# Kernel optimization log

Hardware: AMD Instinct MI355X
Metric: run time of the kernel (lower is better)

The kernel has to match this reference:

```python
import jax, jax.numpy as jnp
import numpy as np
from jax.ops import segment_sum

IN_DIM, HID_DIM, OUT_DIM = 128, 128, 64
N_NODES, N_EDGES = 50000, 800000


def gcn_conv(x, src, dst, W, b, n_nodes):
    # Symmetric GCN normalization (no self loops): deg at targets from unit weights
    deg = segment_sum(jnp.ones(src.shape[0], dtype=x.dtype), dst, num_segments=n_nodes)
    dinv = jnp.where(deg > 0, jax.lax.rsqrt(jnp.maximum(deg, 1.0)), 0.0)
    norm = dinv[src] * dinv[dst]                      # [E]
    h = x @ W                                         # [N, out] small GEMM first (PyG order)
    msg = h[src] * norm[:, None]                      # gather + scale: [E, out]
    out = segment_sum(msg, dst, num_segments=n_nodes) # scatter-add to targets
    return out + b


def setup_inputs() -> dict:
    key = jax.random.key(0)
    k1, k2, k3, k4, k5 = jax.random.split(key, 5)
    x = jax.random.normal(k1, (N_NODES, IN_DIM), dtype=jnp.float32)
    edge_index = jax.random.randint(k2, (2, N_EDGES), 0, N_NODES, dtype=jnp.int64)
    s1 = 1.0 / np.sqrt(IN_DIM)
    s2 = 1.0 / np.sqrt(HID_DIM)
    W1 = jax.random.uniform(k3, (IN_DIM, HID_DIM), jnp.float32, -s1, s1)
    b1 = jnp.zeros((HID_DIM,), jnp.float32)
    W2 = jax.random.uniform(k4, (HID_DIM, OUT_DIM), jnp.float32, -s2, s2)
    b2 = jnp.zeros((OUT_DIM,), jnp.float32)
    return {"x": x, "edge_index": edge_index, "W1": W1, "b1": b1, "W2": W2, "b2": b2}


def reference(x, edge_index, W1, b1, W2, b2):
    n_nodes = x.shape[0]
    src, dst = edge_index[0], edge_index[1]
    h = gcn_conv(x, src, dst, W1, b1, n_nodes)
    h = jax.nn.relu(h)
    # Dropout is identity in eval mode (reference is deterministic)
    out = gcn_conv(h, src, dst, W2, b2, n_nodes)
    return out
```

## Files before the change

kernel.cpp:

```cpp
#include <hip/hip_runtime.h>

#define N_NODES 50000
#define N_EDGES 800000
#define IN_DIM  128
#define HID_DIM 128
#define OUT_DIM 64

#define NPAD 50176
#define NB 7
#define KEYS (N_NODES * NB)
#define KPAD 350208
#define NB_SCAN2 (KPAD / 1024)
#define FILLB ((N_EDGES / 4 + 255) / 256)
#define DINVB ((N_NODES + 1023) / 1024)
#define GEMM1B1024 (NPAD / 256)
#define RANKB (N_EDGES / 256)
#define PREPB 24

typedef __attribute__((ext_vector_type(8))) short bf16x8;
typedef __attribute__((ext_vector_type(4))) float f32x4;

__device__ __forceinline__ unsigned short f2bf(float f) {
    unsigned u = __float_as_uint(f);
    u += 0x7fffu + ((u >> 16) & 1u);
    return (unsigned short)(u >> 16);
}
__device__ __forceinline__ float bflo(unsigned u) { return __uint_as_float(u << 16); }
__device__ __forceinline__ float bfhi(unsigned u) { return __uint_as_float(u & 0xffff0000u); }

#define ACC8(u)  do { \
    acc[0] += bflo(u.x); acc[1] += bfhi(u.x); \
    acc[2] += bflo(u.y); acc[3] += bfhi(u.y); \
    acc[4] += bflo(u.z); acc[5] += bfhi(u.z); \
    acc[6] += bflo(u.w); acc[7] += bfhi(u.w); } while (0)

#define FMA8(u, sc_)  do { \
    acc[0] += bflo(u.x) * (sc_); acc[1] += bfhi(u.x) * (sc_); \
    acc[2] += bflo(u.y) * (sc_); acc[3] += bfhi(u.y) * (sc_); \
    acc[4] += bflo(u.z) * (sc_); acc[5] += bfhi(u.z) * (sc_); \
    acc[6] += bflo(u.w) * (sc_); acc[7] += bfhi(u.w) * (sc_); } while (0)


__global__ __launch_bounds__(256) void prep_rank_kernel(const int* __restrict__ src,
                                                        const int* __restrict__ dst,
                                                        int* __restrict__ cnt2,
                                                        int* __restrict__ rank,
                                                        const float* __restrict__ W1,
                                                        const float* __restrict__ W2,
                                                        unsigned short* __restrict__ w1t,
                                                        unsigned short* __restrict__ w2t) {
    int bid = blockIdx.x;
    int tid = threadIdx.x;
    if (bid < 16) {
        int idx = bid * 256 + tid;
        int c = idx >> 5, k4 = (idx & 31) * 4;
        ushort4 o;
        o.x = f2bf(W1[(k4 + 0) * 128 + c]);
        o.y = f2bf(W1[(k4 + 1) * 128 + c]);
        o.z = f2bf(W1[(k4 + 2) * 128 + c]);
        o.w = f2bf(W1[(k4 + 3) * 128 + c]);
        *(ushort4*)(w1t + c * 128 + k4) = o;
    } else if (bid < PREPB) {
        int idx = (bid - 16) * 256 + tid;
        int c = idx >> 5, k4 = (idx & 31) * 4;
        ushort4 o;
        o.x = f2bf(W2[(k4 + 0) * 64 + c]);
        o.y = f2bf(W2[(k4 + 1) * 64 + c]);
        o.z = f2bf(W2[(k4 + 2) * 64 + c]);
        o.w = f2bf(W2[(k4 + 3) * 64 + c]);
        *(ushort4*)(w2t + c * 128 + k4) = o;
    } else {
        int e = (bid - PREPB) * 256 + tid;
        int s = src[e], d = dst[e];
        rank[e] = atomicAdd(&cnt2[d * NB + (s >> 13)], 1);
    }
}


__global__ __launch_bounds__(1024) void scan_dinv_gemm1_kernel(const int* __restrict__ cnt2,
                                                               int* __restrict__ partials,
                                                               int* __restrict__ rs,
                                                               float* __restrict__ dinv,
                                                               const float* __restrict__ x,
                                                               const unsigned short* __restrict__ w1t,
                                                               unsigned short* __restrict__ h1b) {
    int bid = blockIdx.x;
    int tid = threadIdx.x;
    if (bid < NB_SCAN2) {
        __shared__ int wsum[16];
        __shared__ int woffE[16];
        __shared__ int psum[16];
        __shared__ int bpre;
        int lane = tid & 63, wid = tid >> 6;
        int i = bid * 1024 + tid;
        int v = (i < KEYS) ? cnt2[i] : 0;
        int s = v;
#pragma unroll
        for (int off = 1; off < 64; off <<= 1) {
            int t = __shfl_up(s, off, 64);
            if (lane >= off) s += t;
        }
        if (lane == 63) wsum[wid] = s;
        __syncthreads();
        if (wid == 0) {
            int ws = (lane < 16) ? wsum[lane] : 0;
            int wi = ws;
#pragma unroll
            for (int off = 1; off < 16; off <<= 1) {
                int t = __shfl_up(wi, off, 64);
                if (lane >= off) wi += t;
            }
            if (lane < 16) woffE[lane] = wi - ws;
            if (lane == 15) atomicExch(&partials[bid], wi + 1);
        }
        if (bid == 0 && tid == 0) rs[KEYS] = N_EDGES;
        int myp = 0;
        if (tid < bid) {
            int val;
            do { val = atomicAdd(&partials[tid], 0); } while (val == 0);
            myp = val - 1;
        }
#pragma unroll
        for (int d = 1; d < 64; d <<= 1) myp += __shfl_xor(myp, d, 64);
        if (lane == 0) psum[wid] = myp;
        __syncthreads();
        if (tid == 0) {
            int b = 0;
#pragma unroll
            for (int t = 0; t < 16; ++t) b += psum[t];
            bpre = b;
        }
        __syncthreads();
        if (i < KEYS) rs[i] = bpre + woffE[wid] + s - v;
    } else if (bid < NB_SCAN2 + DINVB) {
        int d = (bid - NB_SCAN2) * 1024 + tid;
        if (d < N_NODES) {
            int base = d * NB;
            int deg = cnt2[base] + cnt2[base + 1] + cnt2[base + 2] + cnt2[base + 3]
                    + cnt2[base + 4] + cnt2[base + 5] + cnt2[base + 6];
            dinv[d] = (deg > 0) ? rsqrtf((float)deg) : 0.0f;
        }
    } else {
        int gb = bid - NB_SCAN2 - DINVB;
        int wave = tid >> 6;
        int lane = tid & 63;
        int n = lane & 15, quad = lane >> 4;
        int row0 = gb * 256 + wave * 16;

        int arow = row0 + n;
        if (arow >= N_NODES) arow = N_NODES - 1;
        const float* aptr = x + (size_t)arow * 128 + quad * 8;
        const unsigned short* bbase = w1t + (size_t)n * 128 + quad * 8;

        f32x4 acc[8];
#pragma unroll
        for (int t = 0; t < 8; ++t) acc[t] = (f32x4){0.f, 0.f, 0.f, 0.f};

#pragma unroll
        for (int w4 = 0; w4 < 4; ++w4) {
            float4 f0 = *(const float4*)(aptr + w4 * 32);
            float4 f1 = *(const float4*)(aptr + w4 * 32 + 4);
            bf16x8 af;
            af[0] = (short)f2bf(f0.x); af[1] = (short)f2bf(f0.y);
            af[2] = (short)f2bf(f0.z); af[3] = (short)f2bf(f0.w);
            af[4] = (short)f2bf(f1.x); af[5] = (short)f2bf(f1.y);
            af[6] = (short)f2bf(f1.z); af[7] = (short)f2bf(f1.w);
#pragma unroll
            for (int t = 0; t < 8; ++t) {
                bf16x8 bf = *(const bf16x8*)(bbase + (size_t)t * 2048 + w4 * 32);
                acc[t] = __builtin_amdgcn_mfma_f32_16x16x32_bf16(af, bf, acc[t], 0, 0, 0);
            }
        }

#pragma unroll
        for (int r = 0; r < 4; ++r) {
            int row = row0 + quad * 4 + r;
            if (row < N_NODES) {
                unsigned short* o = h1b + (size_t)row * 128 + n;
#pragma unroll
                for (int t = 0; t < 8; ++t) o[t * 16] = f2bf(acc[t][r]);
            }
        }
    }
}


__global__ __launch_bounds__(256) void fill_kernel(const int* __restrict__ src,
                                                   const int* __restrict__ dst,
                                                   const int* __restrict__ rank,
                                                   const int* __restrict__ rs,
                                                   int* __restrict__ csr_src) {
    int e = (blockIdx.x * 256 + threadIdx.x) * 4;
    if (e >= N_EDGES) return;
    int4 s4 = *(const int4*)(src + e);
    int4 d4 = *(const int4*)(dst + e);
    int4 r4 = *(const int4*)(rank + e);
    csr_src[rs[d4.x * NB + (s4.x >> 13)] + r4.x] = s4.x;
    csr_src[rs[d4.y * NB + (s4.y >> 13)] + r4.y] = s4.y;
    csr_src[rs[d4.z * NB + (s4.z >> 13)] + r4.z] = s4.z;
    csr_src[rs[d4.w * NB + (s4.w >> 13)] + r4.w] = s4.w;
}


#define A1T_STRIDE 136

__global__ __launch_bounds__(256) void agg1_gemm2_fused(const int* __restrict__ csr_src,
                                                        const int* __restrict__ rs,
                                                        const float* __restrict__ dinv,
                                                        const float* __restrict__ b1,
                                                        const unsigned short* __restrict__ h1b,
                                                        const unsigned short* __restrict__ w2t,
                                                        unsigned short* __restrict__ h2b) {
    __shared__ unsigned short a1t[16 * A1T_STRIDE];

    int node0 = blockIdx.x * 16;
    int g = threadIdx.x >> 4;
    int q = threadIdx.x & 15;
    int node = node0 + g;
    int start = rs[node * NB];
    int m = rs[node * NB + NB] - start;

    float acc[8] = {};
    int j = 0;
    for (; j + 3 < m; j += 4) {
        int s0 = csr_src[start + j];
        int s1 = csr_src[start + j + 1];
        int s2 = csr_src[start + j + 2];
        int s3 = csr_src[start + j + 3];
        float ds0 = dinv[s0];
        float ds1 = dinv[s1];
        float ds2 = dinv[s2];
        float ds3 = dinv[s3];
        uint4 u0 = ((const uint4*)(h1b + (size_t)s0 * 128))[q];
        uint4 u1 = ((const uint4*)(h1b + (size_t)s1 * 128))[q];
        uint4 u2 = ((const uint4*)(h1b + (size_t)s2 * 128))[q];
        uint4 u3 = ((const uint4*)(h1b + (size_t)s3 * 128))[q];
        FMA8(u0, ds0); FMA8(u1, ds1); FMA8(u2, ds2); FMA8(u3, ds3);
    }
    for (; j < m; ++j) {
        int s0 = csr_src[start + j];
        float ds0 = dinv[s0];
        uint4 u0 = ((const uint4*)(h1b + (size_t)s0 * 128))[q];
        FMA8(u0, ds0);
    }

    {
        float dn = dinv[node];
        float4 bA = ((const float4*)b1)[2 * q];
        float4 bB = ((const float4*)b1)[2 * q + 1];
        ushort4 oA, oB;
        oA.x = f2bf(fmaxf(acc[0] * dn + bA.x, 0.f));
        oA.y = f2bf(fmaxf(acc[1] * dn + bA.y, 0.f));
        oA.z = f2bf(fmaxf(acc[2] * dn + bA.z, 0.f));
        oA.w = f2bf(fmaxf(acc[3] * dn + bA.w, 0.f));
        oB.x = f2bf(fmaxf(acc[4] * dn + bB.x, 0.f));
        oB.y = f2bf(fmaxf(acc[5] * dn + bB.y, 0.f));
        oB.z = f2bf(fmaxf(acc[6] * dn + bB.z, 0.f));
        oB.w = f2bf(fmaxf(acc[7] * dn + bB.w, 0.f));
        ushort4* o = (ushort4*)(a1t + g * A1T_STRIDE + q * 8);
        o[0] = oA;
        o[1] = oB;
    }
    __syncthreads();

    int wave = threadIdx.x >> 6;
    int lane = threadIdx.x & 63;
    int n = lane & 15, quad = lane >> 4;
    const unsigned short* bbase = w2t + (size_t)(wave * 16 + n) * 128 + quad * 8;
    const unsigned short* abase = a1t + (size_t)n * A1T_STRIDE + quad * 8;

    f32x4 c2 = (f32x4){0.f, 0.f, 0.f, 0.f};
#pragma unroll
    for (int w4 = 0; w4 < 4; ++w4) {
        bf16x8 af = *(const bf16x8*)(abase + w4 * 32);
        bf16x8 bf = *(const bf16x8*)(bbase + w4 * 32);
        c2 = __builtin_amdgcn_mfma_f32_16x16x32_bf16(af, bf, c2, 0, 0, 0);
    }

#pragma unroll
    for (int r = 0; r < 4; ++r) {
        int row = node0 + quad * 4 + r;
        float dn = dinv[row];
        h2b[(size_t)row * 64 + wave * 16 + n] = f2bf(c2[r] * dn);
    }
}


__global__ __launch_bounds__(256) void agg2_kernel(const int* __restrict__ csr_src,
                                                   const int* __restrict__ rs,
                                                   const float* __restrict__ dinv,
                                                   const float* __restrict__ b2,
                                                   const unsigned short* __restrict__ h2b,
                                                   float* __restrict__ out) {
    int node = blockIdx.x * 4 + (threadIdx.x >> 6);
    if (node >= N_NODES) return;
    int lane = threadIdx.x & 63;
    int grp = lane >> 3;
    int q   = lane & 7;
    int start = rs[node * NB];
    int m = rs[node * NB + NB] - start;

    float acc[8] = {};

    int j = grp;
    for (; j + 8 < m; j += 16) {
        int s0 = csr_src[start + j];
        int s1 = csr_src[start + j + 8];
        uint4 u0 = ((const uint4*)(h2b + (size_t)s0 * 64))[q];
        uint4 u1 = ((const uint4*)(h2b + (size_t)s1 * 64))[q];
        ACC8(u0); ACC8(u1);
    }
    if (j < m) {
        int s0 = csr_src[start + j];
        uint4 u0 = ((const uint4*)(h2b + (size_t)s0 * 64))[q];
        ACC8(u0);
    }

#pragma unroll
    for (int d = 8; d <= 32; d <<= 1) {
#pragma unroll
        for (int c = 0; c < 8; ++c) acc[c] += __shfl_xor(acc[c], d, 64);
    }

    if (lane < 8) {
        float dn = dinv[node];
        float4 bA = ((const float4*)b2)[2 * q];
        float4 bB = ((const float4*)b2)[2 * q + 1];
        float4 rA, rB;
        rA.x = acc[0] * dn + bA.x;
        rA.y = acc[1] * dn + bA.y;
        rA.z = acc[2] * dn + bA.z;
        rA.w = acc[3] * dn + bA.w;
        rB.x = acc[4] * dn + bB.x;
        rB.y = acc[5] * dn + bB.y;
        rB.z = acc[6] * dn + bB.z;
        rB.w = acc[7] * dn + bB.w;
        float4* o = (float4*)(out + (size_t)node * 64);
        o[2 * q] = rA;
        o[2 * q + 1] = rB;
    }
}


extern "C" void kernel_launch(void* const* d_in, const int* in_sizes, int n_in,
                              void* d_out, int out_size, void* d_ws, size_t ws_size,
                              hipStream_t stream) {
    const float* x  = (const float*)d_in[0];
    const int*   ei = (const int*)d_in[1];
    const float* W1 = (const float*)d_in[2];
    const float* b1 = (const float*)d_in[3];
    const float* W2 = (const float*)d_in[4];
    const float* b2 = (const float*)d_in[5];
    float* out = (float*)d_out;

    const int* src = ei;
    const int* dst = ei + N_EDGES;

    char* ws = (char*)d_ws;
    int*   cnt2      = (int*)ws;
    int*   partials  = cnt2 + KPAD;
    int*   rs        = partials + 512;
    float* dinv      = (float*)(rs + KPAD);
    int*   rank      = (int*)(dinv + NPAD);
    int*   csr_src   = rank + N_EDGES;
    unsigned short* h1b = (unsigned short*)(csr_src + N_EDGES);
    unsigned short* h2b = h1b + (size_t)N_NODES * HID_DIM;
    unsigned short* w1t = h2b + (size_t)N_NODES * OUT_DIM;
    unsigned short* w2t = w1t + 128 * 128;

    (void)hipMemsetAsync(cnt2, 0, (KPAD + 512) * sizeof(int), stream);

    prep_rank_kernel<<<PREPB + RANKB, 256, 0, stream>>>(src, dst, cnt2, rank,
                                                        W1, W2, w1t, w2t);

    scan_dinv_gemm1_kernel<<<NB_SCAN2 + DINVB + GEMM1B1024, 1024, 0, stream>>>(
        cnt2, partials, rs, dinv, x, w1t, h1b);

    fill_kernel<<<FILLB, 256, 0, stream>>>(src, dst, rank, rs, csr_src);

    agg1_gemm2_fused<<<N_NODES / 16, 256, 0, stream>>>(csr_src, rs, dinv, b1, h1b, w2t, h2b);

    agg2_kernel<<<(N_NODES + 3) / 4, 256, 0, stream>>>(csr_src, rs, dinv, b2, h2b, out);
}
```

Measured before the change: 212.3 us.

## Move GEMM1 into fill kernel and pre-scale h1 rows by dinv

The first dense GEMM moves out of the scan/dinv kernel into the CSR fill kernel as extra blocks of 64 rows each, so the scan kernel is lighter. Each GEMM1 output row is now multiplied by the source node's dinv before the bf16 store, so layer-1 aggregation no longer gathers dinv per edge and uses plain adds instead of FMAs. This removes 800K random dinv loads from the aggregation loop. The cost is rounding after scaling rather than before, and GEMM1 now has to wait for the scan to finish, which shifts which stages can overlap.

Result: faster. 206.3 us (-2.8%).

```diff
diff --git a/kernel.cpp b/kernel.cpp
--- a/kernel.cpp
+++ b/kernel.cpp
@@ -12,8 +12,8 @@
 #define KPAD 350208
 #define NB_SCAN2 (KPAD / 1024)
 #define FILLB ((N_EDGES / 4 + 255) / 256)
+#define GEMM1B ((N_NODES + 63) / 64)
 #define DINVB ((N_NODES + 1023) / 1024)
-#define GEMM1B1024 (NPAD / 256)
 #define RANKB (N_EDGES / 256)
 #define PREPB 24
 
@@ -33,12 +33,6 @@
     acc[2] += bflo(u.y); acc[3] += bfhi(u.y); \
     acc[4] += bflo(u.z); acc[5] += bfhi(u.z); \
     acc[6] += bflo(u.w); acc[7] += bfhi(u.w); } while (0)
-
-#define FMA8(u, sc_)  do { \
-    acc[0] += bflo(u.x) * (sc_); acc[1] += bfhi(u.x) * (sc_); \
-    acc[2] += bflo(u.y) * (sc_); acc[3] += bfhi(u.y) * (sc_); \
-    acc[4] += bflo(u.z) * (sc_); acc[5] += bfhi(u.z) * (sc_); \
-    acc[6] += bflo(u.w) * (sc_); acc[7] += bfhi(u.w) * (sc_); } while (0)
 
 
 __global__ __launch_bounds__(256) void prep_rank_kernel(const int* __restrict__ src,
@@ -77,13 +71,10 @@
 }
 
 
-__global__ __launch_bounds__(1024) void scan_dinv_gemm1_kernel(const int* __restrict__ cnt2,
-                                                               int* __restrict__ partials,
-                                                               int* __restrict__ rs,
-                                                               float* __restrict__ dinv,
-                                                               const float* __restrict__ x,
-                                                               const unsigned short* __restrict__ w1t,
-                                                               unsigned short* __restrict__ h1b) {
+__global__ __launch_bounds__(1024) void scan_dinv_kernel(const int* __restrict__ cnt2,
+                                                         int* __restrict__ partials,
+                                                         int* __restrict__ rs,
+                                                         float* __restrict__ dinv) {
     int bid = blockIdx.x;
     int tid = threadIdx.x;
     if (bid < NB_SCAN2) {
@@ -132,7 +123,7 @@
         }
         __syncthreads();
         if (i < KEYS) rs[i] = bpre + woffE[wid] + s - v;
-    } else if (bid < NB_SCAN2 + DINVB) {
+    } else {
         int d = (bid - NB_SCAN2) * 1024 + tid;
         if (d < N_NODES) {
             int base = d * NB;
@@ -140,65 +131,74 @@
                     + cnt2[base + 4] + cnt2[base + 5] + cnt2[base + 6];
             dinv[d] = (deg > 0) ? rsqrtf((float)deg) : 0.0f;
         }
-    } else {
-        int gb = bid - NB_SCAN2 - DINVB;
-        int wave = tid >> 6;
-        int lane = tid & 63;
-        int n = lane & 15, quad = lane >> 4;
-        int row0 = gb * 256 + wave * 16;
-
-        int arow = row0 + n;
-        if (arow >= N_NODES) arow = N_NODES - 1;
-        const float* aptr = x + (size_t)arow * 128 + quad * 8;
-        const unsigned short* bbase = w1t + (size_t)n * 128 + quad * 8;
-
-        f32x4 acc[8];
-#pragma unroll
-        for (int t = 0; t < 8; ++t) acc[t] = (f32x4){0.f, 0.f, 0.f, 0.f};
-
-#pragma unroll
-        for (int w4 = 0; w4 < 4; ++w4) {
-            float4 f0 = *(const float4*)(aptr + w4 * 32);
-            float4 f1 = *(const float4*)(aptr + w4 * 32 + 4);
-            bf16x8 af;
-            af[0] = (short)f2bf(f0.x); af[1] = (short)f2bf(f0.y);
-            af[2] = (short)f2bf(f0.z); af[3] = (short)f2bf(f0.w);
-            af[4] = (short)f2bf(f1.x); af[5] = (short)f2bf(f1.y);
-            af[6] = (short)f2bf(f1.z); af[7] = (short)f2bf(f1.w);
-#pragma unroll
-            for (int t = 0; t < 8; ++t) {
-                bf16x8 bf = *(const bf16x8*)(bbase + (size_t)t * 2048 + w4 * 32);
-                acc[t] = __builtin_amdgcn_mfma_f32_16x16x32_bf16(af, bf, acc[t], 0, 0, 0);
-            }
-        }
-
-#pragma unroll
-        for (int r = 0; r < 4; ++r) {
-            int row = row0 + quad * 4 + r;
-            if (row < N_NODES) {
-                unsigned short* o = h1b + (size_t)row * 128 + n;
-#pragma unroll
-                for (int t = 0; t < 8; ++t) o[t * 16] = f2bf(acc[t][r]);
-            }
-        }
-    }
-}
-
-
-__global__ __launch_bounds__(256) void fill_kernel(const int* __restrict__ src,
-                                                   const int* __restrict__ dst,
-                                                   const int* __restrict__ rank,
-                                                   const int* __restrict__ rs,
-                                                   int* __restrict__ csr_src) {
-    int e = (blockIdx.x * 256 + threadIdx.x) * 4;
-    if (e >= N_EDGES) return;
-    int4 s4 = *(const int4*)(src + e);
-    int4 d4 = *(const int4*)(dst + e);
-    int4 r4 = *(const int4*)(rank + e);
-    csr_src[rs[d4.x * NB + (s4.x >> 13)] + r4.x] = s4.x;
-    csr_src[rs[d4.y * NB + (s4.y >> 13)] + r4.y] = s4.y;
-    csr_src[rs[d4.z * NB + (s4.z >> 13)] + r4.z] = s4.z;
-    csr_src[rs[d4.w * NB + (s4.w >> 13)] + r4.w] = s4.w;
+    }
+}
+
+
+__global__ __launch_bounds__(256) void fill_gemm1_kernel(const int* __restrict__ src,
+                                                         const int* __restrict__ dst,
+                                                         const int* __restrict__ rank,
+                                                         const int* __restrict__ rs,
+                                                         int* __restrict__ csr_src,
+                                                         const float* __restrict__ x,
+                                                         const unsigned short* __restrict__ w1t,
+                                                         const float* __restrict__ dinv,
+                                                         unsigned short* __restrict__ h1b) {
+    int bid = blockIdx.x;
+    if (bid < FILLB) {
+        int e = (bid * 256 + threadIdx.x) * 4;
+        if (e >= N_EDGES) return;
+        int4 s4 = *(const int4*)(src + e);
+        int4 d4 = *(const int4*)(dst + e);
+        int4 r4 = *(const int4*)(rank + e);
+        csr_src[rs[d4.x * NB + (s4.x >> 13)] + r4.x] = s4.x;
+        csr_src[rs[d4.y * NB + (s4.y >> 13)] + r4.y] = s4.y;
+        csr_src[rs[d4.z * NB + (s4.z >> 13)] + r4.z] = s4.z;
+        csr_src[rs[d4.w * NB + (s4.w >> 13)] + r4.w] = s4.w;
+        return;
+    }
+
+    int gb = bid - FILLB;
+    int wave = threadIdx.x >> 6;
+    int lane = threadIdx.x & 63;
+    int n = lane & 15, quad = lane >> 4;
+    int row0 = gb * 64 + wave * 16;
+
+    int arow = row0 + n;
+    if (arow >= N_NODES) arow = N_NODES - 1;
+    const float* aptr = x + (size_t)arow * 128 + quad * 8;
+    const unsigned short* bbase = w1t + (size_t)n * 128 + quad * 8;
+
+    f32x4 acc[8];
+#pragma unroll
+    for (int t = 0; t < 8; ++t) acc[t] = (f32x4){0.f, 0.f, 0.f, 0.f};
+
+#pragma unroll
+    for (int w4 = 0; w4 < 4; ++w4) {
+        float4 f0 = *(const float4*)(aptr + w4 * 32);
+        float4 f1 = *(const float4*)(aptr + w4 * 32 + 4);
+        bf16x8 af;
+        af[0] = (short)f2bf(f0.x); af[1] = (short)f2bf(f0.y);
+        af[2] = (short)f2bf(f0.z); af[3] = (short)f2bf(f0.w);
+        af[4] = (short)f2bf(f1.x); af[5] = (short)f2bf(f1.y);
+        af[6] = (short)f2bf(f1.z); af[7] = (short)f2bf(f1.w);
+#pragma unroll
+        for (int t = 0; t < 8; ++t) {
+            bf16x8 bf = *(const bf16x8*)(bbase + (size_t)t * 2048 + w4 * 32);
+            acc[t] = __builtin_amdgcn_mfma_f32_16x16x32_bf16(af, bf, acc[t], 0, 0, 0);
+        }
+    }
+
+#pragma unroll
+    for (int r = 0; r < 4; ++r) {
+        int row = row0 + quad * 4 + r;
+        if (row < N_NODES) {
+            float dn = dinv[row];
+            unsigned short* o = h1b + (size_t)row * 128 + n;
+#pragma unroll
+            for (int t = 0; t < 8; ++t) o[t * 16] = f2bf(acc[t][r] * dn);
+        }
+    }
 }
 
 
@@ -227,21 +227,16 @@
         int s1 = csr_src[start + j + 1];
         int s2 = csr_src[start + j + 2];
         int s3 = csr_src[start + j + 3];
-        float ds0 = dinv[s0];
-        float ds1 = dinv[s1];
-        float ds2 = dinv[s2];
-        float ds3 = dinv[s3];
         uint4 u0 = ((const uint4*)(h1b + (size_t)s0 * 128))[q];
         uint4 u1 = ((const uint4*)(h1b + (size_t)s1 * 128))[q];
         uint4 u2 = ((const uint4*)(h1b + (size_t)s2 * 128))[q];
         uint4 u3 = ((const uint4*)(h1b + (size_t)s3 * 128))[q];
-        FMA8(u0, ds0); FMA8(u1, ds1); FMA8(u2, ds2); FMA8(u3, ds3);
+        ACC8(u0); ACC8(u1); ACC8(u2); ACC8(u3);
     }
     for (; j < m; ++j) {
         int s0 = csr_src[start + j];
-        float ds0 = dinv[s0];
         uint4 u0 = ((const uint4*)(h1b + (size_t)s0 * 128))[q];
-        FMA8(u0, ds0);
+        ACC8(u0);
     }
 
     {
@@ -373,10 +368,10 @@
     prep_rank_kernel<<<PREPB + RANKB, 256, 0, stream>>>(src, dst, cnt2, rank,
                                                         W1, W2, w1t, w2t);
 
-    scan_dinv_gemm1_kernel<<<NB_SCAN2 + DINVB + GEMM1B1024, 1024, 0, stream>>>(
-        cnt2, partials, rs, dinv, x, w1t, h1b);
-
-    fill_kernel<<<FILLB, 256, 0, stream>>>(src, dst, rank, rs, csr_src);
+    scan_dinv_kernel<<<NB_SCAN2 + DINVB, 1024, 0, stream>>>(cnt2, partials, rs, dinv);
+
+    fill_gemm1_kernel<<<FILLB + GEMM1B, 256, 0, stream>>>(src, dst, rank, rs, csr_src,
+                                                          x, w1t, dinv, h1b);
 
     agg1_gemm2_fused<<<N_NODES / 16, 256, 0, stream>>>(csr_src, rs, dinv, b1, h1b, w2t, h2b);
 
```
